# Performance work log

Hardware: AMD Instinct MI355X
Metric: run time of the kernel (lower is better)

The kernel has to match this reference:

```python
import jax, jax.numpy as jnp
import numpy as np

B, S, D, H, DH = 1, 4096, 768, 12, 64
BS = 64            # block size
NB = S // BS       # 64 blocks
R = 3              # random blocks per query block
L = 2              # encoder layers
V = 50358          # vocab
F = 3072           # ffn hidden
C = 8              # num labels
EPS = 1e-12


def _ln(x, w, b):
    mu = jnp.mean(x, -1, keepdims=True)
    var = jnp.var(x, -1, keepdims=True)
    return (x - mu) * jax.lax.rsqrt(var + EPS) * w + b


def _bigbird_attn(x, rand, Wq, bq, Wk, bk, Wv, bv, Wo, bo):
    # x: [B,S,D]; rand: [H,NB,R] int block indices
    def split(h):  # -> [B,H,NB,BS,DH]
        return h.reshape(B, NB, BS, H, DH).transpose(0, 3, 1, 2, 4)
    q = split(x @ Wq + bq)
    k = split(x @ Wk + bk)
    v = split(x @ Wv + bv)
    scale = 1.0 / np.sqrt(DH).astype(np.float32)
    kf = k.reshape(B, H, S, DH)
    vf = v.reshape(B, H, S, DH)
    # global (first/last) query blocks attend to everything
    qe = q[:, :, jnp.array([0, NB - 1])]                       # [B,H,2,BS,DH]
    se = jnp.einsum('bhnqd,bhkd->bhnqk', qe, kf) * scale       # [B,H,2,BS,S]
    oe = jnp.einsum('bhnqk,bhkd->bhnqd', jax.nn.softmax(se, -1), vf)
    # middle query blocks: global(0, NB-1) + sliding window + R random blocks
    mid = jnp.arange(1, NB - 1)                                # [M]
    win = jnp.stack([jnp.zeros_like(mid), jnp.full_like(mid, NB - 1),
                     mid - 1, mid, mid + 1], -1)               # [M,5]
    band = jnp.concatenate([jnp.broadcast_to(win, (H, NB - 2, 5)),
                            rand[:, 1:NB - 1]], -1)            # [H,M,W]
    Wn = band.shape[-1]
    hidx = jnp.arange(H)[:, None, None]
    kb = k[:, hidx, band].reshape(B, H, NB - 2, Wn * BS, DH)
    vb = v[:, hidx, band].reshape(B, H, NB - 2, Wn * BS, DH)
    sm = jnp.einsum('bhmqd,bhmkd->bhmqk', q[:, :, 1:NB - 1], kb) * scale
    om = jnp.einsum('bhmqk,bhmkd->bhmqd', jax.nn.softmax(sm, -1), vb)
    o = jnp.concatenate([oe[:, :, 0:1], om, oe[:, :, 1:2]], 2)  # [B,H,NB,BS,DH]
    o = o.transpose(0, 2, 3, 1, 4).reshape(B, S, D)
    return o @ Wo + bo


def _forward(input_ids, rand_attn, word_emb, pos_emb, emb_ln_w, emb_ln_b,
             Wq, bq, Wk, bk, Wv, bv, Wo, bo, ln1_w, ln1_b,
             W1, b1, W2, b2, ln2_w, ln2_b, Wc, bc):
    h = word_emb[input_ids] + pos_emb[None, :S]
    h = _ln(h, emb_ln_w, emb_ln_b)
    for l in range(L):
        a = _bigbird_attn(h, rand_attn[l], Wq[l], bq[l], Wk[l], bk[l],
                          Wv[l], bv[l], Wo[l], bo[l])
        h = _ln(h + a, ln1_w[l], ln1_b[l])
        f = jax.nn.gelu(h @ W1[l] + b1[l], approximate=True) @ W2[l] + b2[l]
        h = _ln(h + f, ln2_w[l], ln2_b[l])
    return h[:, -1, :] @ Wc + bc   # [B, C]


def setup_inputs() -> dict:
    key = jax.random.key(0)
    ks = jax.random.split(key, 24)
    std = 0.02
    d = {
        'input_ids': jax.random.randint(ks[0], (B, S), 0, V, dtype=jnp.int32),
        'rand_attn': jax.random.randint(ks[1], (L, H, NB, R), 0, NB, dtype=jnp.int32),
        'word_emb': jax.random.normal(ks[2], (V, D), jnp.float32) * std,
        'pos_emb': jax.random.normal(ks[3], (S, D), jnp.float32) * std,
        'emb_ln_w': jnp.ones((D,), jnp.float32),
        'emb_ln_b': jnp.zeros((D,), jnp.float32),
        'Wq': jax.random.normal(ks[4], (L, D, D), jnp.float32) * std,
        'bq': jnp.zeros((L, D), jnp.float32),
        'Wk': jax.random.normal(ks[5], (L, D, D), jnp.float32) * std,
        'bk': jnp.zeros((L, D), jnp.float32),
        'Wv': jax.random.normal(ks[6], (L, D, D), jnp.float32) * std,
        'bv': jnp.zeros((L, D), jnp.float32),
        'Wo': jax.random.normal(ks[7], (L, D, D), jnp.float32) * std,
        'bo': jnp.zeros((L, D), jnp.float32),
        'ln1_w': jnp.ones((L, D), jnp.float32),
        'ln1_b': jnp.zeros((L, D), jnp.float32),
        'W1': jax.random.normal(ks[8], (L, D, F), jnp.float32) * std,
        'b1': jnp.zeros((L, F), jnp.float32),
        'W2': jax.random.normal(ks[9], (L, F, D), jnp.float32) * std,
        'b2': jnp.zeros((L, D), jnp.float32),
        'ln2_w': jnp.ones((L, D), jnp.float32),
        'ln2_b': jnp.zeros((L, D), jnp.float32),
        'Wc': jax.random.normal(ks[10], (D, C), jnp.float32) * std,
        'bc': jnp.zeros((C,), jnp.float32),
    }
    return d


def reference(input_ids, rand_attn, word_emb, pos_emb, emb_ln_w, emb_ln_b,
              Wq, bq, Wk, bk, Wv, bv, Wo, bo, ln1_w, ln1_b,
              W1, b1, W2, b2, ln2_w, ln2_b, Wc, bc):
    return _forward(input_ids, rand_attn, word_emb, pos_emb, emb_ln_w, emb_ln_b,
                    Wq, bq, Wk, bk, Wv, bv, Wo, bo, ln1_w, ln1_b,
                    W1, b1, W2, b2, ln2_w, ln2_b, Wc, bc)
```

## Files before the change

### kernel.cpp

```cpp
#include <hip/hip_runtime.h>
#include <stdint.h>

#define S_LEN 4096
#define DMODEL 768
#define NHEAD 12
#define DHEAD 64
#define NBLK 64
#define FF 3072
#define NLAYER 2
#define NMID (NHEAD * (NBLK - 2))
#define NEDGE_WG (NHEAD * 2 * 8)

typedef __attribute__((ext_vector_type(8))) short short8;
typedef __attribute__((ext_vector_type(4))) float floatx4;
typedef unsigned short ushort_t;

__device__ __forceinline__ unsigned short f2bf(float f) {
    union { float f; unsigned u; } v; v.f = f;
    unsigned r = v.u + 0x7FFFu + ((v.u >> 16) & 1u);
    return (unsigned short)(r >> 16);
}

__device__ __forceinline__ float fast_gelu(float v) {
    float u = 0.7978845608f * (v + 0.044715f * v * v * v);
    float e = __expf(2.0f * u);
    float th = 1.0f - 2.0f / (e + 1.0f);
    return 0.5f * v * (1.0f + th);
}

__device__ __forceinline__ void load_lds16(const void* g, void* l) {
    __builtin_amdgcn_global_load_lds((const __attribute__((address_space(1))) void*)g,
                                     (__attribute__((address_space(3))) void*)l, 16, 0, 0);
}

__global__ void embed_ln_kernel(const int* __restrict__ ids, const float* __restrict__ wemb,
                                const float* __restrict__ pemb, const float* __restrict__ w,
                                const float* __restrict__ b, float* __restrict__ hf,
                                ushort_t* __restrict__ hb) {
    int s = blockIdx.x, t = threadIdx.x;
    const float* we = wemb + (size_t)ids[s] * DMODEL;
    const float* pe = pemb + (size_t)s * DMODEL;
    float x0 = we[t] + pe[t];
    float x1 = we[t + 256] + pe[t + 256];
    float x2 = we[t + 512] + pe[t + 512];
    float sum = x0 + x1 + x2;
    float sum2 = x0 * x0 + x1 * x1 + x2 * x2;
    __shared__ float sred[8];
    for (int o = 32; o >= 1; o >>= 1) { sum += __shfl_down(sum, o); sum2 += __shfl_down(sum2, o); }
    if ((t & 63) == 0) { sred[t >> 6] = sum; sred[4 + (t >> 6)] = sum2; }
    __syncthreads();
    float ts = sred[0] + sred[1] + sred[2] + sred[3];
    float ts2 = sred[4] + sred[5] + sred[6] + sred[7];
    float mu = ts * (1.0f / DMODEL);
    float rs = rsqrtf(ts2 * (1.0f / DMODEL) - mu * mu + 1e-12f);
    size_t base = (size_t)s * DMODEL;
    float y0 = (x0 - mu) * rs * w[t] + b[t];
    float y1 = (x1 - mu) * rs * w[t + 256] + b[t + 256];
    float y2 = (x2 - mu) * rs * w[t + 512] + b[t + 512];
    hf[base + t] = y0; hf[base + t + 256] = y1; hf[base + t + 512] = y2;
    hb[base + t] = f2bf(y0); hb[base + t + 256] = f2bf(y1); hb[base + t + 512] = f2bf(y2);
}

__global__ void ln_kernel(const float* __restrict__ in, const float* __restrict__ w,
                          const float* __restrict__ b, float* __restrict__ hf,
                          ushort_t* __restrict__ hb) {
    int s = blockIdx.x, t = threadIdx.x;
    const float* row = in + (size_t)s * DMODEL;
    float x0 = row[t], x1 = row[t + 256], x2 = row[t + 512];
    float sum = x0 + x1 + x2;
    float sum2 = x0 * x0 + x1 * x1 + x2 * x2;
    __shared__ float sred[8];
    for (int o = 32; o >= 1; o >>= 1) { sum += __shfl_down(sum, o); sum2 += __shfl_down(sum2, o); }
    if ((t & 63) == 0) { sred[t >> 6] = sum; sred[4 + (t >> 6)] = sum2; }
    __syncthreads();
    float ts = sred[0] + sred[1] + sred[2] + sred[3];
    float ts2 = sred[4] + sred[5] + sred[6] + sred[7];
    float mu = ts * (1.0f / DMODEL);
    float rs = rsqrtf(ts2 * (1.0f / DMODEL) - mu * mu + 1e-12f);
    size_t base = (size_t)s * DMODEL;
    float y0 = (x0 - mu) * rs * w[t] + b[t];
    float y1 = (x1 - mu) * rs * w[t + 256] + b[t + 256];
    float y2 = (x2 - mu) * rs * w[t + 512] + b[t + 512];
    hf[base + t] = y0; hf[base + t + 256] = y1; hf[base + t + 512] = y2;
    hb[base + t] = f2bf(y0); hb[base + t + 256] = f2bf(y1); hb[base + t + 512] = f2bf(y2);
}

__global__ void transpose_all(const float* __restrict__ Wq, const float* __restrict__ Wk,
                              const float* __restrict__ Wv, const float* __restrict__ Wo,
                              const float* __restrict__ W1, const float* __restrict__ W2,
                              ushort_t* __restrict__ WqkvT, ushort_t* __restrict__ WoT,
                              ushort_t* __restrict__ W1T, ushort_t* __restrict__ W2T) {
    __shared__ float tile[32][33];
    int b = blockIdx.x;
    const float* src; ushort_t* dst; int K, N, bx;
    if (b < 2304) {
        int m = b / 576, r = b % 576;
        src = (m == 0) ? Wq : (m == 1) ? Wk : (m == 2) ? Wv : Wo;
        dst = (m < 3) ? (WqkvT + (size_t)m * DMODEL * DMODEL) : WoT;
        K = DMODEL; N = DMODEL; bx = r;
    } else if (b < 4608) {
        src = W1; dst = W1T; K = DMODEL; N = FF; bx = b - 2304;
    } else {
        src = W2; dst = W2T; K = FF; N = DMODEL; bx = b - 4608;
    }
    int gx = N / 32;
    int n0 = (bx % gx) * 32, k0 = (bx / gx) * 32;
    int tx = threadIdx.x, ty = threadIdx.y;
    for (int i = 0; i < 32; i += 8)
        tile[ty + i][tx] = src[(size_t)(k0 + ty + i) * N + n0 + tx];
    __syncthreads();
    for (int i = 0; i < 32; i += 8)
        dst[(size_t)(n0 + ty + i) * K + k0 + tx] = f2bf(tile[tx][ty + i]);
}

template <int MODE>
__global__ __launch_bounds__(256, 2) void gemm_bf16(
    const ushort_t* __restrict__ A, const ushort_t* __restrict__ BT,
    int M, int N, int K,
    const float* __restrict__ bias, const float* __restrict__ resid,
    float* __restrict__ outf, ushort_t* __restrict__ outb,
    ushort_t* __restrict__ qout, ushort_t* __restrict__ kout, ushort_t* __restrict__ vout,
    const float* __restrict__ bq, const float* __restrict__ bk, const float* __restrict__ bv) {
    __shared__ __align__(16) ushort_t Asm[128 * 64];
    __shared__ __align__(16) ushort_t Bsm[128 * 64];
    int tid = threadIdx.x;
    int lane = tid & 63, wave = tid >> 6;
    int quad = lane >> 4, l16 = lane & 15;
    int wm = wave >> 1, wn = wave & 1;
    long arow0 = (long)blockIdx.y * 128;
    long bcol0 = (long)blockIdx.x * 128;
    int r8 = lane >> 3;
    int gchunk = (lane & 7) ^ (r8 & 7);
    const ushort_t* agp0 = A + (arow0 + r8) * (long)K + gchunk * 8;
    const ushort_t* bgp0 = BT + (bcol0 + r8) * (long)K + gchunk * 8;
    floatx4 acc[4][4];
#pragma unroll
    for (int i = 0; i < 4; i++)
#pragma unroll
        for (int j = 0; j < 4; j++) acc[i][j] = (floatx4){0.f, 0.f, 0.f, 0.f};

    for (int k0 = 0; k0 < K; k0 += 64) {
        __syncthreads();
#pragma unroll
        for (int t2 = 0; t2 < 4; t2++) {
            int seg = wave * 4 + t2;
            load_lds16(agp0 + (long)seg * 8 * K + k0, Asm + seg * 512);
            load_lds16(bgp0 + (long)seg * 8 * K + k0, Bsm + seg * 512);
        }
        __syncthreads();
#pragma unroll
        for (int ks = 0; ks < 2; ks++) {
            short8 af[4], bfv[4];
#pragma unroll
            for (int i = 0; i < 4; i++)
                af[i] = *(const short8*)&Asm[(wm * 64 + i * 16 + l16) * 64 +
                                             (((ks * 4 + quad) ^ (l16 & 7)) * 8)];
#pragma unroll
            for (int j = 0; j < 4; j++)
                bfv[j] = *(const short8*)&Bsm[(wn * 64 + j * 16 + l16) * 64 +
                                              (((ks * 4 + quad) ^ (l16 & 7)) * 8)];
#pragma unroll
            for (int i = 0; i < 4; i++)
#pragma unroll
                for (int j = 0; j < 4; j++)
                    acc[i][j] = __builtin_amdgcn_mfma_f32_16x16x32_bf16(af[i], bfv[j], acc[i][j], 0, 0, 0);
        }
    }

#pragma unroll
    for (int i = 0; i < 4; i++) {
        long row = arow0 + wm * 64 + i * 16 + quad * 4;
#pragma unroll
        for (int j = 0; j < 4; j++) {
            long col = bcol0 + wn * 64 + j * 16 + l16;
#pragma unroll
            for (int r = 0; r < 4; r++) {
                float v = acc[i][j][r];
                long rw = row + r;
                if (MODE == 0) {
                    int n = (int)col;
                    if (n < DMODEL) {
                        v = (v + bq[n]) * 0.125f;
                        int hh = n >> 6, dh = n & 63;
                        qout[((long)hh * S_LEN + rw) * DHEAD + dh] = f2bf(v);
                    } else if (n < 2 * DMODEL) {
                        int n2 = n - DMODEL; v += bk[n2];
                        int hh = n2 >> 6, dh = n2 & 63;
                        kout[((long)hh * S_LEN + rw) * DHEAD + dh] = f2bf(v);
                    } else {
                        int n2 = n - 2 * DMODEL; v += bv[n2];
                        int hh = n2 >> 6, dh = n2 & 63;
                        vout[((long)hh * S_LEN + rw) * DHEAD + dh] = f2bf(v);
                    }
                } else if (MODE == 1) {
                    v += bias[col] + resid[rw * (long)N + col];
                    outf[rw * (long)N + col] = v;
                } else {
                    v += bias[col];
                    outb[rw * (long)N + col] = f2bf(fast_gelu(v));
                }
            }
        }
    }
}

__global__ __launch_bounds__(256, 2) void attn_kernel(
    const ushort_t* __restrict__ qb, const ushort_t* __restrict__ kb,
    const ushort_t* __restrict__ vb, const int* __restrict__ randl,
    ushort_t* __restrict__ out, float* __restrict__ opart, float* __restrict__ mlpart) {
    __shared__ __align__(16) ushort_t Ks[64 * 72];
    __shared__ __align__(16) ushort_t Vs[64 * 72];
    __shared__ __align__(16) ushort_t Ps[4][16 * 72];
    __shared__ int kls[8];
    int tid = threadIdx.x, lane = tid & 63, wave = tid >> 6, quad = lane >> 4, l16 = lane & 15;
    int g = blockIdx.x;
    int h, qblk, chunk = 0, eidx = 0;
    bool mid;
    if (g < NMID) {
        mid = true;
        h = g / (NBLK - 2);
        qblk = 1 + g % (NBLK - 2);
    } else {
        mid = false;
        int t = g - NMID;
        int side = t / (NHEAD * 8);
        int t2 = t % (NHEAD * 8);
        h = t2 >> 3;
        chunk = t2 & 7;
        qblk = side ? (NBLK - 1) : 0;
        eidx = side * NHEAD + h;
    }
    if (mid && tid < 8) {
        int v;
        if (tid == 0) v = 0;
        else if (tid == 1) v = NBLK - 1;
        else if (tid == 2) v = qblk - 1;
        else if (tid == 3) v = qblk;
        else if (tid == 4) v = qblk + 1;
        else v = randl[(h * NBLK + qblk) * 3 + (tid - 5)];
        kls[tid] = v;
    }
    const ushort_t* qh = qb + (size_t)h * S_LEN * DHEAD;
    const ushort_t* kh = kb + (size_t)h * S_LEN * DHEAD;
    const ushort_t* vh = vb + (size_t)h * S_LEN * DHEAD;
    size_t qoff = ((size_t)(qblk * 64 + wave * 16 + l16)) * DHEAD;
    short8 qf0 = *(const short8*)&qh[qoff + quad * 8];
    short8 qf1 = *(const short8*)&qh[qoff + 32 + quad * 8];
    floatx4 oacc[4];
#pragma unroll
    for (int j = 0; j < 4; j++) oacc[j] = (floatx4){0.f, 0.f, 0.f, 0.f};
    float mrun[4] = {-1e30f, -1e30f, -1e30f, -1e30f};
    float lrun[4] = {0.f, 0.f, 0.f, 0.f};

    for (int it = 0; it < 8; ++it) {
        __syncthreads();
        int kbi = mid ? kls[it] : (chunk * 8 + it);
        {
            const ushort_t* src = kh + (size_t)kbi * 64 * DHEAD;
#pragma unroll
            for (int c = 0; c < 2; c++) {
                int chk = tid + c * 256;
                int krow = chk >> 3, kc = chk & 7;
                *(uint4*)&Ks[krow * 72 + kc * 8] = *(const uint4*)&src[chk * 8];
            }
            const ushort_t* vsrc = vh + (size_t)kbi * 64 * DHEAD;
#pragma unroll
            for (int c = 0; c < 2; c++) {
                int dh0 = wave * 16 + c * 8;
                uint4 d4 = *(const uint4*)&vsrc[lane * DHEAD + dh0];
                const ushort_t* e = (const ushort_t*)&d4;
#pragma unroll
                for (int j = 0; j < 8; j++) Vs[(dh0 + j) * 72 + lane] = e[j];
            }
        }
        __syncthreads();
        floatx4 sacc[4];
#pragma unroll
        for (int jt = 0; jt < 4; jt++) {
            short8 kf0 = *(const short8*)&Ks[(jt * 16 + l16) * 72 + quad * 8];
            short8 kf1 = *(const short8*)&Ks[(jt * 16 + l16) * 72 + 32 + quad * 8];
            floatx4 z = (floatx4){0.f, 0.f, 0.f, 0.f};
            z = __builtin_amdgcn_mfma_f32_16x16x32_bf16(qf0, kf0, z, 0, 0, 0);
            z = __builtin_amdgcn_mfma_f32_16x16x32_bf16(qf1, kf1, z, 0, 0, 0);
            sacc[jt] = z;
        }
#pragma unroll
        for (int r = 0; r < 4; r++) {
            float mx = fmaxf(fmaxf(sacc[0][r], sacc[1][r]), fmaxf(sacc[2][r], sacc[3][r]));
#pragma unroll
            for (int o = 1; o < 16; o <<= 1) mx = fmaxf(mx, __shfl_xor(mx, o));
            float mnew = fmaxf(mrun[r], mx);
            float al = __expf(mrun[r] - mnew);
            float pv[4], ps = 0.f;
#pragma unroll
            for (int jt = 0; jt < 4; jt++) { pv[jt] = __expf(sacc[jt][r] - mnew); ps += pv[jt]; }
#pragma unroll
            for (int o = 1; o < 16; o <<= 1) ps += __shfl_xor(ps, o);
            lrun[r] = lrun[r] * al + ps;
            mrun[r] = mnew;
#pragma unroll
            for (int jt = 0; jt < 4; jt++) {
                oacc[jt][r] *= al;
                Ps[wave][(quad * 4 + r) * 72 + jt * 16 + l16] = f2bf(pv[jt]);
            }
        }
        short8 pa0 = *(const short8*)&Ps[wave][l16 * 72 + quad * 8];
        short8 pa1 = *(const short8*)&Ps[wave][l16 * 72 + 32 + quad * 8];
#pragma unroll
        for (int jt = 0; jt < 4; jt++) {
            short8 vf0 = *(const short8*)&Vs[(jt * 16 + l16) * 72 + quad * 8];
            short8 vf1 = *(const short8*)&Vs[(jt * 16 + l16) * 72 + 32 + quad * 8];
            oacc[jt] = __builtin_amdgcn_mfma_f32_16x16x32_bf16(pa0, vf0, oacc[jt], 0, 0, 0);
            oacc[jt] = __builtin_amdgcn_mfma_f32_16x16x32_bf16(pa1, vf1, oacc[jt], 0, 0, 0);
        }
    }
    if (mid) {
#pragma unroll
        for (int jt = 0; jt < 4; jt++)
#pragma unroll
            for (int r = 0; r < 4; r++) {
                int row = qblk * 64 + wave * 16 + quad * 4 + r;
                int col = h * DHEAD + jt * 16 + l16;
                out[(size_t)row * DMODEL + col] = f2bf(oacc[jt][r] / lrun[r]);
            }
    } else {
        float* op = opart + ((size_t)(eidx * 8 + chunk)) * 64 * 64;
        float* ml = mlpart + ((size_t)(eidx * 8 + chunk)) * 64 * 2;
#pragma unroll
        for (int jt = 0; jt < 4; jt++)
#pragma unroll
            for (int r = 0; r < 4; r++) {
                int row = wave * 16 + quad * 4 + r;
                op[(size_t)row * 64 + jt * 16 + l16] = oacc[jt][r];
            }
        if (l16 == 0) {
#pragma unroll
            for (int r = 0; r < 4; r++) {
                int row = wave * 16 + quad * 4 + r;
                ml[row * 2 + 0] = mrun[r];
                ml[row * 2 + 1] = lrun[r];
            }
        }
    }
}

__global__ void attn_combine(const float* __restrict__ opart, const float* __restrict__ mlpart,
                             ushort_t* __restrict__ out) {
    int e = blockIdx.x;
    int side = e / NHEAD, h = e % NHEAD;
    int qblk = side ? (NBLK - 1) : 0;
    __shared__ float mls[8][64][2];
    int tid = threadIdx.x;
    for (int i = tid; i < 8 * 64 * 2; i += 256)
        ((float*)mls)[i] = mlpart[(size_t)e * 8 * 64 * 2 + i];
    __syncthreads();
    int col = tid & 63, r0 = (tid >> 6) * 16;
    const float* ope = opart + (size_t)e * 8 * 64 * 64;
    for (int row = r0; row < r0 + 16; ++row) {
        float M = -1e30f;
#pragma unroll
        for (int p = 0; p < 8; p++) M = fmaxf(M, mls[p][row][0]);
        float L = 0.f, O = 0.f;
#pragma unroll
        for (int p = 0; p < 8; p++) {
            float al = __expf(mls[p][row][0] - M);
            L += mls[p][row][1] * al;
            O += ope[((size_t)p * 64 + row) * 64 + col] * al;
        }
        out[(size_t)(qblk * 64 + row) * DMODEL + h * DHEAD + col] = f2bf(O / L);
    }
}

__global__ void classifier_kernel(const float* __restrict__ hf, const float* __restrict__ Wc,
                                  const float* __restrict__ bc, float* __restrict__ out) {
    int t = threadIdx.x;
    int c = t & 7, seg = t >> 3;
    const float* hr = hf + (size_t)(S_LEN - 1) * DMODEL;
    float p = 0.f;
    for (int i = 0; i < 24; i++) { int d = seg * 24 + i; p += hr[d] * Wc[d * 8 + c]; }
    __shared__ float red[256];
    red[t] = p;
    __syncthreads();
    for (int o = 128; o >= 8; o >>= 1) { if (t < o) red[t] += red[t + o]; __syncthreads(); }
    if (t < 8) out[t] = red[t] + bc[t];
}

extern "C" void kernel_launch(void* const* d_in, const int* in_sizes, int n_in,
                              void* d_out, int out_size, void* d_ws, size_t ws_size,
                              hipStream_t stream) {
    (void)in_sizes; (void)n_in; (void)out_size; (void)ws_size;
    const int* input_ids = (const int*)d_in[0];
    const int* rand_attn = (const int*)d_in[1];
    const float* word_emb = (const float*)d_in[2];
    const float* pos_emb = (const float*)d_in[3];
    const float* emb_ln_w = (const float*)d_in[4];
    const float* emb_ln_b = (const float*)d_in[5];
    const float* Wq = (const float*)d_in[6];
    const float* bq = (const float*)d_in[7];
    const float* Wk = (const float*)d_in[8];
    const float* bk = (const float*)d_in[9];
    const float* Wv = (const float*)d_in[10];
    const float* bv = (const float*)d_in[11];
    const float* Wo = (const float*)d_in[12];
    const float* bo = (const float*)d_in[13];
    const float* ln1_w = (const float*)d_in[14];
    const float* ln1_b = (const float*)d_in[15];
    const float* W1 = (const float*)d_in[16];
    const float* b1 = (const float*)d_in[17];
    const float* W2 = (const float*)d_in[18];
    const float* b2 = (const float*)d_in[19];
    const float* ln2_w = (const float*)d_in[20];
    const float* ln2_b = (const float*)d_in[21];
    const float* Wc = (const float*)d_in[22];
    const float* bc = (const float*)d_in[23];
    float* outp = (float*)d_out;

    char* ws = (char*)d_ws;
    size_t off = 0;
    auto alloc = [&](size_t bytes) -> void* {
        void* p = ws + off;
        off += (bytes + 255) & ~(size_t)255;
        return p;
    };
    float* hf = (float*)alloc((size_t)S_LEN * DMODEL * 4);
    ushort_t* hb = (ushort_t*)alloc((size_t)S_LEN * DMODEL * 2);
    float* res = (float*)alloc((size_t)S_LEN * DMODEL * 4);
    ushort_t* WqkvT = (ushort_t*)alloc((size_t)3 * DMODEL * DMODEL * 2);
    ushort_t* WoT = (ushort_t*)alloc((size_t)DMODEL * DMODEL * 2);
    ushort_t* W1T = (ushort_t*)alloc((size_t)FF * DMODEL * 2);
    ushort_t* W2T = (ushort_t*)alloc((size_t)DMODEL * FF * 2);
    ushort_t* qbuf = (ushort_t*)alloc((size_t)NHEAD * S_LEN * DHEAD * 2);
    ushort_t* kbuf = (ushort_t*)alloc((size_t)NHEAD * S_LEN * DHEAD * 2);
    ushort_t* vbuf = (ushort_t*)alloc((size_t)NHEAD * S_LEN * DHEAD * 2);
    ushort_t* attnb = (ushort_t*)alloc((size_t)S_LEN * DMODEL * 2);
    ushort_t* gbuf = (ushort_t*)alloc((size_t)S_LEN * FF * 2);
    float* opart = (float*)alloc((size_t)24 * 8 * 64 * 64 * 4);
    float* mlpart = (float*)alloc((size_t)24 * 8 * 64 * 2 * 4);

    dim3 blk256(256);
    dim3 tb(32, 8);

    embed_ln_kernel<<<S_LEN, blk256, 0, stream>>>(input_ids, word_emb, pos_emb,
                                                  emb_ln_w, emb_ln_b, hf, hb);

    for (int l = 0; l < NLAYER; ++l) {
        const float* Wq_l = Wq + (size_t)l * DMODEL * DMODEL;
        const float* Wk_l = Wk + (size_t)l * DMODEL * DMODEL;
        const float* Wv_l = Wv + (size_t)l * DMODEL * DMODEL;
        const float* Wo_l = Wo + (size_t)l * DMODEL * DMODEL;
        const float* W1_l = W1 + (size_t)l * DMODEL * FF;
        const float* W2_l = W2 + (size_t)l * FF * DMODEL;
        const float* bq_l = bq + (size_t)l * DMODEL;
        const float* bk_l = bk + (size_t)l * DMODEL;
        const float* bv_l = bv + (size_t)l * DMODEL;
        const float* bo_l = bo + (size_t)l * DMODEL;
        const float* b1_l = b1 + (size_t)l * FF;
        const float* b2_l = b2 + (size_t)l * DMODEL;
        const float* ln1w_l = ln1_w + (size_t)l * DMODEL;
        const float* ln1b_l = ln1_b + (size_t)l * DMODEL;
        const float* ln2w_l = ln2_w + (size_t)l * DMODEL;
        const float* ln2b_l = ln2_b + (size_t)l * DMODEL;
        const int* rand_l = rand_attn + (size_t)l * NHEAD * NBLK * 3;

        transpose_all<<<6912, tb, 0, stream>>>(Wq_l, Wk_l, Wv_l, Wo_l, W1_l, W2_l,
                                               WqkvT, WoT, W1T, W2T);

        gemm_bf16<0><<<dim3(3 * DMODEL / 128, S_LEN / 128), blk256, 0, stream>>>(
            hb, WqkvT, S_LEN, 3 * DMODEL, DMODEL,
            nullptr, nullptr, nullptr, nullptr, qbuf, kbuf, vbuf, bq_l, bk_l, bv_l);

        attn_kernel<<<NMID + NEDGE_WG, blk256, 0, stream>>>(qbuf, kbuf, vbuf, rand_l,
                                                            attnb, opart, mlpart);
        attn_combine<<<24, blk256, 0, stream>>>(opart, mlpart, attnb);

        gemm_bf16<1><<<dim3(DMODEL / 128, S_LEN / 128), blk256, 0, stream>>>(
            attnb, WoT, S_LEN, DMODEL, DMODEL,
            bo_l, hf, res, nullptr, nullptr, nullptr, nullptr, nullptr, nullptr, nullptr);

        ln_kernel<<<S_LEN, blk256, 0, stream>>>(res, ln1w_l, ln1b_l, hf, hb);

        gemm_bf16<2><<<dim3(FF / 128, S_LEN / 128), blk256, 0, stream>>>(
            hb, W1T, S_LEN, FF, DMODEL,
            b1_l, nullptr, nullptr, gbuf, nullptr, nullptr, nullptr, nullptr, nullptr, nullptr);

        gemm_bf16<1><<<dim3(DMODEL / 128, S_LEN / 128), blk256, 0, stream>>>(
            gbuf, W2T, S_LEN, DMODEL, FF,
            b2_l, hf, res, nullptr, nullptr, nullptr, nullptr, nullptr, nullptr, nullptr);

        ln_kernel<<<S_LEN, blk256, 0, stream>>>(res, ln2w_l, ln2b_l, hf, hb);
    }

    classifier_kernel<<<1, blk256, 0, stream>>>(hf, Wc, bc, outp);
}
```

Baseline: 680.4 us.

## Split-K the narrow output GEMMs with atomics and batch weight transposes

The Wo and W2 projections (N=768) now use split-K across gridDim.z (2 and 4 slices) and accumulate with float atomicAdd into a residual buffer. A separate init kernel pre-fills that buffer with bias plus residual. This raises workgroup count from 192 to 384 or 768 so the GPU's CUs are filled better. Weight transposes for both layers are also merged into a single launch before the loop. The cost is extra atomic traffic, an extra elementwise pass, and non-deterministic summation order.

```diff
diff --git a/kernel.cpp b/kernel.cpp
--- a/kernel.cpp
+++ b/kernel.cpp
@@ -85,6 +85,16 @@
     hb[base + t] = f2bf(y0); hb[base + t + 256] = f2bf(y1); hb[base + t + 512] = f2bf(y2);
 }
 
+__global__ void init_addbias(const float* __restrict__ bias, const float* __restrict__ resid,
+                             float* __restrict__ out, int Nq) {
+    int idx = blockIdx.x * 256 + threadIdx.x;
+    int col4 = idx % Nq;
+    float4 b4 = *(const float4*)&bias[col4 * 4];
+    float4 r4 = ((const float4*)resid)[idx];
+    float4 o4 = {r4.x + b4.x, r4.y + b4.y, r4.z + b4.z, r4.w + b4.w};
+    ((float4*)out)[idx] = o4;
+}
+
 __global__ void transpose_all(const float* __restrict__ Wq, const float* __restrict__ Wk,
                               const float* __restrict__ Wv, const float* __restrict__ Wo,
                               const float* __restrict__ W1, const float* __restrict__ W2,
@@ -92,16 +102,21 @@
                               ushort_t* __restrict__ W1T, ushort_t* __restrict__ W2T) {
     __shared__ float tile[32][33];
     int b = blockIdx.x;
+    int layer = b / 6912;
+    b %= 6912;
+    size_t lwo = (size_t)layer * DMODEL * DMODEL;
+    size_t lwf = (size_t)layer * DMODEL * FF;
     const float* src; ushort_t* dst; int K, N, bx;
     if (b < 2304) {
         int m = b / 576, r = b % 576;
-        src = (m == 0) ? Wq : (m == 1) ? Wk : (m == 2) ? Wv : Wo;
-        dst = (m < 3) ? (WqkvT + (size_t)m * DMODEL * DMODEL) : WoT;
+        src = ((m == 0) ? Wq : (m == 1) ? Wk : (m == 2) ? Wv : Wo) + lwo;
+        dst = (m < 3) ? (WqkvT + (size_t)layer * 3 * DMODEL * DMODEL + (size_t)m * DMODEL * DMODEL)
+                      : (WoT + (size_t)layer * DMODEL * DMODEL);
         K = DMODEL; N = DMODEL; bx = r;
     } else if (b < 4608) {
-        src = W1; dst = W1T; K = DMODEL; N = FF; bx = b - 2304;
+        src = W1 + lwf; dst = W1T + (size_t)layer * DMODEL * FF; K = DMODEL; N = FF; bx = b - 2304;
     } else {
-        src = W2; dst = W2T; K = FF; N = DMODEL; bx = b - 4608;
+        src = W2 + lwf; dst = W2T + (size_t)layer * DMODEL * FF; K = FF; N = DMODEL; bx = b - 4608;
     }
     int gx = N / 32;
     int n0 = (bx % gx) * 32, k0 = (bx / gx) * 32;
@@ -129,6 +144,8 @@
     int wm = wave >> 1, wn = wave & 1;
     long arow0 = (long)blockIdx.y * 128;
     long bcol0 = (long)blockIdx.x * 128;
+    int kper = K / gridDim.z;
+    int kbeg = blockIdx.z * kper, kend = kbeg + kper;
     int r8 = lane >> 3;
     int gchunk = (lane & 7) ^ (r8 & 7);
     const ushort_t* agp0 = A + (arow0 + r8) * (long)K + gchunk * 8;
@@ -139,7 +156,7 @@
 #pragma unroll
         for (int j = 0; j < 4; j++) acc[i][j] = (floatx4){0.f, 0.f, 0.f, 0.f};
 
-    for (int k0 = 0; k0 < K; k0 += 64) {
+    for (int k0 = kbeg; k0 < kend; k0 += 64) {
         __syncthreads();
 #pragma unroll
         for (int t2 = 0; t2 < 4; t2++) {
@@ -192,12 +209,11 @@
                         int hh = n2 >> 6, dh = n2 & 63;
                         vout[((long)hh * S_LEN + rw) * DHEAD + dh] = f2bf(v);
                     }
-                } else if (MODE == 1) {
-                    v += bias[col] + resid[rw * (long)N + col];
-                    outf[rw * (long)N + col] = v;
-                } else {
+                } else if (MODE == 2) {
                     v += bias[col];
                     outb[rw * (long)N + col] = f2bf(fast_gelu(v));
+                } else {
+                    atomicAdd(&outf[rw * (long)N + col], v);
                 }
             }
         }
@@ -425,10 +441,10 @@
     float* hf = (float*)alloc((size_t)S_LEN * DMODEL * 4);
     ushort_t* hb = (ushort_t*)alloc((size_t)S_LEN * DMODEL * 2);
     float* res = (float*)alloc((size_t)S_LEN * DMODEL * 4);
-    ushort_t* WqkvT = (ushort_t*)alloc((size_t)3 * DMODEL * DMODEL * 2);
-    ushort_t* WoT = (ushort_t*)alloc((size_t)DMODEL * DMODEL * 2);
-    ushort_t* W1T = (ushort_t*)alloc((size_t)FF * DMODEL * 2);
-    ushort_t* W2T = (ushort_t*)alloc((size_t)DMODEL * FF * 2);
+    ushort_t* WqkvT = (ushort_t*)alloc((size_t)NLAYER * 3 * DMODEL * DMODEL * 2);
+    ushort_t* WoT = (ushort_t*)alloc((size_t)NLAYER * DMODEL * DMODEL * 2);
+    ushort_t* W1T = (ushort_t*)alloc((size_t)NLAYER * FF * DMODEL * 2);
+    ushort_t* W2T = (ushort_t*)alloc((size_t)NLAYER * DMODEL * FF * 2);
     ushort_t* qbuf = (ushort_t*)alloc((size_t)NHEAD * S_LEN * DHEAD * 2);
     ushort_t* kbuf = (ushort_t*)alloc((size_t)NHEAD * S_LEN * DHEAD * 2);
     ushort_t* vbuf = (ushort_t*)alloc((size_t)NHEAD * S_LEN * DHEAD * 2);
@@ -442,14 +458,14 @@
 
     embed_ln_kernel<<<S_LEN, blk256, 0, stream>>>(input_ids, word_emb, pos_emb,
                                                   emb_ln_w, emb_ln_b, hf, hb);
+    transpose_all<<<NLAYER * 6912, tb, 0, stream>>>(Wq, Wk, Wv, Wo, W1, W2,
+                                                    WqkvT, WoT, W1T, W2T);
 
     for (int l = 0; l < NLAYER; ++l) {
-        const float* Wq_l = Wq + (size_t)l * DMODEL * DMODEL;
-        const float* Wk_l = Wk + (size_t)l * DMODEL * DMODEL;
-        const float* Wv_l = Wv + (size_t)l * DMODEL * DMODEL;
-        const float* Wo_l = Wo + (size_t)l * DMODEL * DMODEL;
-        const float* W1_l = W1 + (size_t)l * DMODEL * FF;
-        const float* W2_l = W2 + (size_t)l * FF * DMODEL;
+        const ushort_t* WqkvT_l = WqkvT + (size_t)l * 3 * DMODEL * DMODEL;
+        const ushort_t* WoT_l = WoT + (size_t)l * DMODEL * DMODEL;
+        const ushort_t* W1T_l = W1T + (size_t)l * FF * DMODEL;
+        const ushort_t* W2T_l = W2T + (size_t)l * DMODEL * FF;
         const float* bq_l = bq + (size_t)l * DMODEL;
         const float* bk_l = bk + (size_t)l * DMODEL;
         const float* bv_l = bv + (size_t)l * DMODEL;
@@ -462,30 +478,29 @@
         const float* ln2b_l = ln2_b + (size_t)l * DMODEL;
         const int* rand_l = rand_attn + (size_t)l * NHEAD * NBLK * 3;
 
-        transpose_all<<<6912, tb, 0, stream>>>(Wq_l, Wk_l, Wv_l, Wo_l, W1_l, W2_l,
-                                               WqkvT, WoT, W1T, W2T);
-
-        gemm_bf16<0><<<dim3(3 * DMODEL / 128, S_LEN / 128), blk256, 0, stream>>>(
-            hb, WqkvT, S_LEN, 3 * DMODEL, DMODEL,
+        gemm_bf16<0><<<dim3(3 * DMODEL / 128, S_LEN / 128, 1), blk256, 0, stream>>>(
+            hb, WqkvT_l, S_LEN, 3 * DMODEL, DMODEL,
             nullptr, nullptr, nullptr, nullptr, qbuf, kbuf, vbuf, bq_l, bk_l, bv_l);
 
         attn_kernel<<<NMID + NEDGE_WG, blk256, 0, stream>>>(qbuf, kbuf, vbuf, rand_l,
                                                             attnb, opart, mlpart);
         attn_combine<<<24, blk256, 0, stream>>>(opart, mlpart, attnb);
 
-        gemm_bf16<1><<<dim3(DMODEL / 128, S_LEN / 128), blk256, 0, stream>>>(
-            attnb, WoT, S_LEN, DMODEL, DMODEL,
-            bo_l, hf, res, nullptr, nullptr, nullptr, nullptr, nullptr, nullptr, nullptr);
+        init_addbias<<<S_LEN * DMODEL / 4 / 256, blk256, 0, stream>>>(bo_l, hf, res, DMODEL / 4);
+        gemm_bf16<3><<<dim3(DMODEL / 128, S_LEN / 128, 2), blk256, 0, stream>>>(
+            attnb, WoT_l, S_LEN, DMODEL, DMODEL,
+            nullptr, nullptr, res, nullptr, nullptr, nullptr, nullptr, nullptr, nullptr, nullptr);
 
         ln_kernel<<<S_LEN, blk256, 0, stream>>>(res, ln1w_l, ln1b_l, hf, hb);
 
-        gemm_bf16<2><<<dim3(FF / 128, S_LEN / 128), blk256, 0, stream>>>(
-            hb, W1T, S_LEN, FF, DMODEL,
+        gemm_bf16<2><<<dim3(FF / 128, S_LEN / 128, 1), blk256, 0, stream>>>(
+            hb, W1T_l, S_LEN, FF, DMODEL,
             b1_l, nullptr, nullptr, gbuf, nullptr, nullptr, nullptr, nullptr, nullptr, nullptr);
 
-        gemm_bf16<1><<<dim3(DMODEL / 128, S_LEN / 128), blk256, 0, stream>>>(
-            gbuf, W2T, S_LEN, DMODEL, FF,
-            b2_l, hf, res, nullptr, nullptr, nullptr, nullptr, nullptr, nullptr, nullptr);
+        init_addbias<<<S_LEN * DMODEL / 4 / 256, blk256, 0, stream>>>(b2_l, hf, res, DMODEL / 4);
+        gemm_bf16<3><<<dim3(DMODEL / 128, S_LEN / 128, 4), blk256, 0, stream>>>(
+            gbuf, W2T_l, S_LEN, DMODEL, FF,
+            nullptr, nullptr, res, nullptr, nullptr, nullptr, nullptr, nullptr, nullptr, nullptr);
 
         ln_kernel<<<S_LEN, blk256, 0, stream>>>(res, ln2w_l, ln2b_l, hf, hb);
     }
```

Measured after the change: 720.4 us. +5.9%, slower.
